# Kernel optimization log

Hardware: AMD Instinct MI355X
Metric: run time of the kernel (lower is better)

Reference implementation:

```python
import jax, jax.numpy as jnp
import numpy as np

N = 100000
F_IN = 128
F_OUT = 128
NNZ = 1_600_000  # avg degree 16


def spmm(rows, cols, vals, X, n):
    """Sparse [n,n] (COO: rows, cols, vals) times dense X [n,d] -> [n,d]."""
    return jax.ops.segment_sum(vals[:, None] * X[cols], rows, num_segments=n)


def setup_inputs() -> dict:
    key = jax.random.key(0)
    ks = jax.random.split(key, 8)
    x = jax.random.normal(ks[0], (N, F_IN), dtype=jnp.float32)
    W = jax.random.normal(ks[1], (F_IN, F_OUT), dtype=jnp.float32) * 0.05
    kernel = jnp.ones((N, 1), dtype=jnp.float32)  # tf.ones_initializer
    phi0_rows = jax.random.randint(ks[2], (NNZ,), 0, N, dtype=jnp.int64)
    phi0_cols = jax.random.randint(ks[3], (NNZ,), 0, N, dtype=jnp.int64)
    phi0_vals = jax.random.uniform(ks[4], (NNZ,), dtype=jnp.float32)
    phi1_rows = jax.random.randint(ks[5], (NNZ,), 0, N, dtype=jnp.int64)
    phi1_cols = jax.random.randint(ks[6], (NNZ,), 0, N, dtype=jnp.int64)
    phi1_vals = jax.random.uniform(ks[7], (NNZ,), dtype=jnp.float32)
    return {
        "x": x, "W": W, "kernel": kernel,
        "phi0_rows": phi0_rows, "phi0_cols": phi0_cols, "phi0_vals": phi0_vals,
        "phi1_rows": phi1_rows, "phi1_cols": phi1_cols, "phi1_vals": phi1_vals,
    }


def reference(x, W, kernel, phi0_rows, phi0_cols, phi0_vals,
              phi1_rows, phi1_cols, phi1_vals):
    # X' = x @ W  (dense feature projection)
    X_prime = x @ W  # [N, F_OUT]
    # X'_t = phi0 @ X'  (SpMM with wavelet basis)
    X_t = spmm(phi0_rows, phi0_cols, phi0_vals, X_prime, N)
    # out = phi1 @ (kernel * X'_t)  (elementwise spectral scaling then SpMM)
    out = spmm(phi1_rows, phi1_cols, phi1_vals, kernel * X_t, N)
    return jax.nn.relu(out)
```

## Files before the change

kernel.cpp:

```cpp
#include <hip/hip_runtime.h>


constexpr int kN = 100000;
constexpr int kF = 128;
constexpr int kNNZ = 1600000;

constexpr int kBuckets = (kN + 255) / 256;
constexpr int kBucketCap = 4608;
constexpr int kChunk = 7168;
constexpr int kChunkBlocks = (kNNZ + kChunk - 1) / kChunk;
constexpr int kSlotsPerMat = kChunkBlocks * kChunk;
constexpr int kDirStride = kBuckets + 1;
constexpr int kTransBlocks = 64;
constexpr int kGemmBlocks = (kN + 127) / 128;
constexpr int kSpmmBlocks512 = kN * 32 / 512;
constexpr int kRowBlocks = kN * 32 / 256;

typedef short bf16x8 __attribute__((ext_vector_type(8)));
typedef float f32x4 __attribute__((ext_vector_type(4)));
typedef unsigned short ushort4v __attribute__((ext_vector_type(4)));

__device__ __forceinline__ unsigned short f32_to_bf16(float f) {
    unsigned int u = __float_as_uint(f);
    u += 0x7fffu + ((u >> 16) & 1u);
    return (unsigned short)(u >> 16);
}
__device__ __forceinline__ float bf16_to_f32(unsigned short h) {
    return __uint_as_float((unsigned int)h << 16);
}

__global__ __launch_bounds__(256) void scatter_transpose(
    const float* __restrict__ W, unsigned short* __restrict__ Wt,
    const int* __restrict__ r0, const int* __restrict__ c0, const float* __restrict__ v0,
    const int* __restrict__ r1, const int* __restrict__ c1, const float* __restrict__ v1,
    unsigned long long* __restrict__ stg, unsigned short* __restrict__ dir) {
    const int t = threadIdx.x;
    if (blockIdx.x < kTransBlocks) {
        const int e = blockIdx.x * 256 + t;
        const int n = e & 127, k = e >> 7;
        Wt[n * 128 + k] = f32_to_bf16(W[e]);
        return;
    }

    __shared__ unsigned long long recs[kChunk];
    __shared__ int hist[kDirStride];
    __shared__ int cur[kDirStride];
    __shared__ int sc2[256];

    const int b = blockIdx.x - kTransBlocks;
    const bool m1 = b >= kChunkBlocks;
    const int cb = m1 ? b - kChunkBlocks : b;
    const int* rows = m1 ? r1 : r0;
    const int* cols = m1 ? c1 : c0;
    const float* vals = m1 ? v1 : v0;
    unsigned long long* dst = stg + (size_t)b * kChunk;
    unsigned short* dirm = dir + (size_t)b * kDirStride;

    for (int i = t; i < kDirStride; i += 256) hist[i] = 0;
    __syncthreads();

    const int base0 = cb * kChunk;
    const int cnt = min(kNNZ - base0, kChunk);

    for (int j = t; j < cnt; j += 256) atomicAdd(&hist[rows[base0 + j] >> 8], 1);
    __syncthreads();

    int s = 0;
    if (t < 196) s = hist[2 * t] + hist[2 * t + 1];
    sc2[t] = (t < 196) ? s : 0;
    __syncthreads();
    #pragma unroll
    for (int off = 1; off < 256; off <<= 1) {
        const int add = (t >= off) ? sc2[t - off] : 0;
        __syncthreads();
        sc2[t] += add;
        __syncthreads();
    }
    if (t < 196) {
        const int ex = sc2[t] - s;
        cur[2 * t] = ex;
        cur[2 * t + 1] = ex + hist[2 * t];
        dirm[2 * t] = (unsigned short)ex;
        dirm[2 * t + 1] = (unsigned short)(ex + hist[2 * t]);
    }
    __syncthreads();

    for (int j = t; j < cnt; j += 256) {
        const int idx = base0 + j;
        const int r = rows[idx];
        const int bk = r >> 8;
        const int pos = atomicAdd(&cur[bk], 1);
        const unsigned int key = ((unsigned int)(r & 255) << 17) | (unsigned int)cols[idx];
        recs[pos] = ((unsigned long long)__float_as_uint(vals[idx]) << 32) | key;
    }
    __syncthreads();

    for (int j = t; j < cnt; j += 256) dst[j] = recs[j];
}

__device__ __forceinline__ void sort_bucket_body(
    char* smem, int bk, int matSel,
    const unsigned long long* __restrict__ stg,
    const unsigned short* __restrict__ dir,
    unsigned long long* __restrict__ sortedG,
    int* __restrict__ rs, int* __restrict__ re) {
    unsigned long long* sorted = (unsigned long long*)smem;
    int* rlen = (int*)(smem + 36864);
    int* gst  = (int*)(smem + 36864 + 896);
    int* hist = (int*)(smem + 36864 + 1792);
    int* sc   = (int*)(smem + 36864 + 2816);
    int* cur  = (int*)(smem + 36864 + 3840);

    const int t = threadIdx.x;
    const unsigned long long* stgm = stg + (matSel ? (size_t)kSlotsPerMat : 0);

    if (t < kChunkBlocks) {
        const unsigned short* dd =
            dir + (size_t)(matSel * kChunkBlocks + t) * kDirStride;
        const int s = dd[bk];
        rlen[t] = dd[bk + 1] - s;
        gst[t] = t * kChunk + s;
    }
    if (t < 256) hist[t] = 0;
    __syncthreads();

    const int g = t >> 5;
    const int lane = t & 31;

    for (int blk = g; blk < kChunkBlocks; blk += 16) {
        const int len = rlen[blk];
        const int gs = gst[blk];
        for (int i = lane; i < len; i += 32) {
            const unsigned int lo = (unsigned int)stgm[gs + i];
            atomicAdd(&hist[(lo >> 17) & 255], 1);
        }
    }
    __syncthreads();

    const int v = (t < 256) ? hist[t] : 0;
    if (t < 256) sc[t] = v;
    __syncthreads();
    #pragma unroll
    for (int off = 1; off < 256; off <<= 1) {
        const int add = (t < 256 && t >= off) ? sc[t - off] : 0;
        __syncthreads();
        if (t < 256) sc[t] += add;
        __syncthreads();
    }
    if (t < 256) cur[t] = sc[t] - v;
    __syncthreads();

    for (int blk = g; blk < kChunkBlocks; blk += 16) {
        const int len = rlen[blk];
        const int gs = gst[blk];
        for (int i = lane; i < len; i += 32) {
            const unsigned long long p = stgm[gs + i];
            const int lrow = (int)(((unsigned int)p >> 17) & 255);
            sorted[atomicAdd(&cur[lrow], 1)] = p;
        }
    }
    __syncthreads();

    const int nrec = sc[255];
    const int bidx = matSel * kBuckets + bk;
    const size_t outBase = (size_t)bidx * kBucketCap;
    for (int j = t; j < nrec; j += 512) sortedG[outBase + j] = sorted[j];
    if (t < 256) {
        const int row = bk * 256 + t;
        if (row < kN) {
            const int rg = matSel * kN + row;
            rs[rg] = (int)outBase + sc[t] - hist[t];
            re[rg] = (int)outBase + sc[t];
        }
    }
}

template <bool ROW_SCALE, bool RELU, bool OUT_BF16>
__device__ __forceinline__ void spmm_row_body(
    int r, int lane,
    const int* __restrict__ rs, const int* __restrict__ re,
    const unsigned long long* __restrict__ rec,
    const float* __restrict__ scale,
    const unsigned short* __restrict__ Xin,
    void* __restrict__ Xout) {
    const int s = rs[r];
    const int e = re[r];

    float4 acc = make_float4(0.f, 0.f, 0.f, 0.f);

    for (int base = s; base < e; base += 32) {
        int cl = 0;
        float vl = 0.f;
        if (base + lane < e) {
            const unsigned long long p = __builtin_nontemporal_load(&rec[base + lane]);
            cl = (int)((unsigned int)p & 0x1FFFF);
            vl = __uint_as_float((unsigned int)(p >> 32));
        }
        const int m4 = (min(32, e - base) + 3) & ~3;
        for (int j = 0; j < m4; j += 4) {
            const int c0 = __shfl(cl, j, 32);
            const int c1 = __shfl(cl, j + 1, 32);
            const int c2 = __shfl(cl, j + 2, 32);
            const int c3 = __shfl(cl, j + 3, 32);
            const float w0 = __shfl(vl, j, 32);
            const float w1 = __shfl(vl, j + 1, 32);
            const float w2 = __shfl(vl, j + 2, 32);
            const float w3 = __shfl(vl, j + 3, 32);
            const ushort4v x0 = *(const ushort4v*)(Xin + (size_t)c0 * kF + lane * 4);
            const ushort4v x1 = *(const ushort4v*)(Xin + (size_t)c1 * kF + lane * 4);
            const ushort4v x2 = *(const ushort4v*)(Xin + (size_t)c2 * kF + lane * 4);
            const ushort4v x3 = *(const ushort4v*)(Xin + (size_t)c3 * kF + lane * 4);
            acc.x = fmaf(w0, bf16_to_f32(x0.x), acc.x);
            acc.y = fmaf(w0, bf16_to_f32(x0.y), acc.y);
            acc.z = fmaf(w0, bf16_to_f32(x0.z), acc.z);
            acc.w = fmaf(w0, bf16_to_f32(x0.w), acc.w);
            acc.x = fmaf(w1, bf16_to_f32(x1.x), acc.x);
            acc.y = fmaf(w1, bf16_to_f32(x1.y), acc.y);
            acc.z = fmaf(w1, bf16_to_f32(x1.z), acc.z);
            acc.w = fmaf(w1, bf16_to_f32(x1.w), acc.w);
            acc.x = fmaf(w2, bf16_to_f32(x2.x), acc.x);
            acc.y = fmaf(w2, bf16_to_f32(x2.y), acc.y);
            acc.z = fmaf(w2, bf16_to_f32(x2.z), acc.z);
            acc.w = fmaf(w2, bf16_to_f32(x2.w), acc.w);
            acc.x = fmaf(w3, bf16_to_f32(x3.x), acc.x);
            acc.y = fmaf(w3, bf16_to_f32(x3.y), acc.y);
            acc.z = fmaf(w3, bf16_to_f32(x3.z), acc.z);
            acc.w = fmaf(w3, bf16_to_f32(x3.w), acc.w);
        }
    }
    if (ROW_SCALE) {
        const float k = scale[r];
        acc.x *= k; acc.y *= k; acc.z *= k; acc.w *= k;
    }
    if (RELU) {
        acc.x = fmaxf(acc.x, 0.f); acc.y = fmaxf(acc.y, 0.f);
        acc.z = fmaxf(acc.z, 0.f); acc.w = fmaxf(acc.w, 0.f);
    }
    if (OUT_BF16) {
        ushort4v o;
        o.x = f32_to_bf16(acc.x); o.y = f32_to_bf16(acc.y);
        o.z = f32_to_bf16(acc.z); o.w = f32_to_bf16(acc.w);
        __builtin_nontemporal_store(
            o, (ushort4v*)((unsigned short*)Xout + (size_t)r * kF + lane * 4));
    } else {
        f32x4 o;
        o.x = acc.x; o.y = acc.y; o.z = acc.z; o.w = acc.w;
        __builtin_nontemporal_store(o, (f32x4*)Xout + (size_t)r * 32 + lane);
    }
}

__global__ __launch_bounds__(512) void sort_gemm(
    const unsigned long long* __restrict__ stg,
    const unsigned short* __restrict__ dir,
    unsigned long long* __restrict__ sortedG,
    int* __restrict__ rs, int* __restrict__ re,
    const float* __restrict__ x, const unsigned short* __restrict__ Wt,
    unsigned short* __restrict__ Xpb) {
    __shared__ __align__(16) char smem[41728];
    const int t = threadIdx.x;

    if (blockIdx.x < kBuckets) {
        sort_bucket_body(smem, blockIdx.x, 0, stg, dir, sortedG, rs, re);
    } else {
        unsigned short* xs = (unsigned short*)smem;
        const int rowBase = (blockIdx.x - kBuckets) * 128;

        {
            const int lrow = t >> 2;
            const int q = t & 3;
            int srow = rowBase + lrow;
            if (srow >= kN) srow = kN - 1;
            const float4* xr = (const float4*)(x + (size_t)srow * kF) + q * 8;
            #pragma unroll
            for (int i = 0; i < 8; ++i) {
                const float4 f = xr[i];
                ushort4v h;
                h.x = f32_to_bf16(f.x); h.y = f32_to_bf16(f.y);
                h.z = f32_to_bf16(f.z); h.w = f32_to_bf16(f.w);
                const int kidx = q * 32 + i * 4;
                *(ushort4v*)&xs[lrow * 128 + (kidx ^ ((lrow & 7) << 3))] = h;
            }
        }
        __syncthreads();

        const int w = t >> 6;
        const int l = t & 63;
        const int lr = l & 15;
        const int lq = l >> 4;

        f32x4 acc[8];
        #pragma unroll
        for (int n = 0; n < 8; ++n) acc[n] = (f32x4){0.f, 0.f, 0.f, 0.f};

        const int arow = w * 16 + lr;
        #pragma unroll
        for (int ks = 0; ks < 4; ++ks) {
            const int akidx = ks * 32 + lq * 8;
            const bf16x8 a = *(const bf16x8*)&xs[arow * 128 + (akidx ^ ((arow & 7) << 3))];
            #pragma unroll
            for (int n = 0; n < 8; ++n) {
                const int bn = n * 16 + lr;
                const bf16x8 b = *(const bf16x8*)(Wt + bn * 128 + akidx);
                acc[n] = __builtin_amdgcn_mfma_f32_16x16x32_bf16(a, b, acc[n], 0, 0, 0);
            }
        }

        #pragma unroll
        for (int j = 0; j < 4; ++j) {
            const int row = rowBase + w * 16 + lq * 4 + j;
            if (row < kN) {
                unsigned short* orow = Xpb + (size_t)row * kF + lr;
                #pragma unroll
                for (int n = 0; n < 8; ++n) orow[n * 16] = f32_to_bf16(acc[n][j]);
            }
        }
    }
}

__global__ __launch_bounds__(512) void sort_spmm(
    const unsigned long long* __restrict__ stg,
    const unsigned short* __restrict__ dir,
    unsigned long long* __restrict__ sortedG,
    int* __restrict__ rs, int* __restrict__ re,
    const float* __restrict__ kern,
    const unsigned short* __restrict__ Xpb,
    unsigned short* __restrict__ Xtb) {
    __shared__ __align__(16) char smem[41728];

    if (blockIdx.x < kBuckets) {
        sort_bucket_body(smem, blockIdx.x, 1, stg, dir, sortedG, rs, re);
    } else {
        const int t = threadIdx.x;
        const int r = (blockIdx.x - kBuckets) * 16 + (t >> 5);
        spmm_row_body<true, false, true>(r, t & 31, rs, re, sortedG, kern, Xpb, Xtb);
    }
}

__global__ __launch_bounds__(256) void spmm_csr(const int* __restrict__ rs,
                                                const int* __restrict__ re,
                                                const unsigned long long* __restrict__ rec,
                                                const unsigned short* __restrict__ Xin,
                                                float* __restrict__ Xout) {
    const int tid = blockIdx.x * 256 + threadIdx.x;
    spmm_row_body<false, true, false>(tid >> 5, tid & 31, rs, re, rec, nullptr,
                                      Xin, Xout);
}

extern "C" void kernel_launch(void* const* d_in, const int* in_sizes, int n_in,
                              void* d_out, int out_size, void* d_ws, size_t ws_size,
                              hipStream_t stream) {
    const float* x    = (const float*)d_in[0];
    const float* W    = (const float*)d_in[1];
    const float* kern = (const float*)d_in[2];
    const int*   p0r  = (const int*)d_in[3];
    const int*   p0c  = (const int*)d_in[4];
    const float* p0v  = (const float*)d_in[5];
    const int*   p1r  = (const int*)d_in[6];
    const int*   p1c  = (const int*)d_in[7];
    const float* p1v  = (const float*)d_in[8];

    unsigned long long* stg = (unsigned long long*)d_out;

    char* w = (char*)d_ws;
    size_t off = 0;
    unsigned short* Xpb = (unsigned short*)(w + off); off += (size_t)kN * kF * 2;
    unsigned short* Xtb = (unsigned short*)(w + off); off += (size_t)kN * kF * 2;
    unsigned short* Wt = (unsigned short*)(w + off);  off += 128 * 128 * 2;
    unsigned short* dir = (unsigned short*)(w + off);
    off += (size_t)2 * kChunkBlocks * kDirStride * 2;
    off = (off + 15) & ~(size_t)15;
    unsigned long long* sortedG = (unsigned long long*)(w + off);
    off += (size_t)2 * kBuckets * kBucketCap * 8;
    int* rs = (int*)(w + off);                        off += (size_t)2 * kN * 4;
    int* re = (int*)(w + off);                        off += (size_t)2 * kN * 4;

    scatter_transpose<<<kTransBlocks + 2 * kChunkBlocks, 256, 0, stream>>>(
        W, Wt, p0r, p0c, p0v, p1r, p1c, p1v, stg, dir);

    sort_gemm<<<kBuckets + kGemmBlocks, 512, 0, stream>>>(
        stg, dir, sortedG, rs, re, x, Wt, Xpb);

    sort_spmm<<<kBuckets + kSpmmBlocks512, 512, 0, stream>>>(
        stg, dir, sortedG, rs, re, kern, Xpb, Xtb);

    spmm_csr<<<kRowBlocks, 256, 0, stream>>>(rs + kN, re + kN, sortedG, Xtb,
                                             (float*)d_out);
}
```

Before: 205.4 us.

## Slice feature matrices into 16-column panels and pack sparse records to 32 bits

The dense intermediates are stored as 8 feature slices of 16 bf16 columns, each contiguous over rows. Each SpMM block now handles one slice for 64 rows, with 8 lanes per row, so that concurrently running blocks gather from a smaller working set with better cache locality. Sparse records shrink from 64-bit (fp32 value) to 32-bit (17-bit column plus fp16 value), halving index traffic. The cost is fp16 rounding of the matrix values, eightfold rereads of the row pointers and records, and narrower 4-byte gathers.

```diff
diff --git a/kernel.cpp b/kernel.cpp
--- a/kernel.cpp
+++ b/kernel.cpp
@@ -1,4 +1,5 @@
 #include <hip/hip_runtime.h>
+#include <hip/hip_fp16.h>
 
 
 constexpr int kN = 100000;
@@ -13,8 +14,10 @@
 constexpr int kDirStride = kBuckets + 1;
 constexpr int kTransBlocks = 64;
 constexpr int kGemmBlocks = (kN + 127) / 128;
-constexpr int kSpmmBlocks512 = kN * 32 / 512;
-constexpr int kRowBlocks = kN * 32 / 256;
+constexpr int kSliceN = 8;
+constexpr int kSliceF = 16;
+constexpr int kSpmmRowGroups = (kN + 63) / 64;
+constexpr int kSpmmBlocksSM = kSliceN * kSpmmRowGroups;
 
 typedef short bf16x8 __attribute__((ext_vector_type(8)));
 typedef float f32x4 __attribute__((ext_vector_type(4)));
@@ -24,9 +27,6 @@
     unsigned int u = __float_as_uint(f);
     u += 0x7fffu + ((u >> 16) & 1u);
     return (unsigned short)(u >> 16);
-}
-__device__ __forceinline__ float bf16_to_f32(unsigned short h) {
-    return __uint_as_float((unsigned int)h << 16);
 }
 
 __global__ __launch_bounds__(256) void scatter_transpose(
@@ -102,7 +102,7 @@
     char* smem, int bk, int matSel,
     const unsigned long long* __restrict__ stg,
     const unsigned short* __restrict__ dir,
-    unsigned long long* __restrict__ sortedG,
+    unsigned int* __restrict__ sortedG,
     int* __restrict__ rs, int* __restrict__ re) {
     unsigned long long* sorted = (unsigned long long*)smem;
     int* rlen = (int*)(smem + 36864);
@@ -164,7 +164,13 @@
     const int nrec = sc[255];
     const int bidx = matSel * kBuckets + bk;
     const size_t outBase = (size_t)bidx * kBucketCap;
-    for (int j = t; j < nrec; j += 512) sortedG[outBase + j] = sorted[j];
+    for (int j = t; j < nrec; j += 512) {
+        const unsigned long long p = sorted[j];
+        const unsigned int col = (unsigned int)p & 0x1FFFFu;
+        const float vv = __uint_as_float((unsigned int)(p >> 32));
+        const unsigned short h = __half_as_ushort(__float2half(vv));
+        sortedG[outBase + j] = col | ((unsigned int)h << 17);
+    }
     if (t < 256) {
         const int row = bk * 256 + t;
         if (row < kN) {
@@ -176,83 +182,69 @@
 }
 
 template <bool ROW_SCALE, bool RELU, bool OUT_BF16>
-__device__ __forceinline__ void spmm_row_body(
-    int r, int lane,
+__device__ __forceinline__ void spmm_slice_body(
+    int slice, int rowBase, int t,
     const int* __restrict__ rs, const int* __restrict__ re,
-    const unsigned long long* __restrict__ rec,
+    const unsigned int* __restrict__ rec,
     const float* __restrict__ scale,
-    const unsigned short* __restrict__ Xin,
+    const unsigned short* __restrict__ Xsm,
     void* __restrict__ Xout) {
-    const int s = rs[r];
-    const int e = re[r];
-
-    float4 acc = make_float4(0.f, 0.f, 0.f, 0.f);
-
-    for (int base = s; base < e; base += 32) {
+    const int r = rowBase + (t >> 3);
+    if (r >= kN) return;
+    const int lane8 = t & 7;
+    const int s0 = rs[r];
+    const int e0 = re[r];
+    const unsigned short* Xs = Xsm + (size_t)slice * kN * kSliceF;
+
+    float a0 = 0.f, a1 = 0.f;
+    for (int base = s0; base < e0; base += 8) {
         int cl = 0;
         float vl = 0.f;
-        if (base + lane < e) {
-            const unsigned long long p = __builtin_nontemporal_load(&rec[base + lane]);
-            cl = (int)((unsigned int)p & 0x1FFFF);
-            vl = __uint_as_float((unsigned int)(p >> 32));
-        }
-        const int m4 = (min(32, e - base) + 3) & ~3;
-        for (int j = 0; j < m4; j += 4) {
-            const int c0 = __shfl(cl, j, 32);
-            const int c1 = __shfl(cl, j + 1, 32);
-            const int c2 = __shfl(cl, j + 2, 32);
-            const int c3 = __shfl(cl, j + 3, 32);
-            const float w0 = __shfl(vl, j, 32);
-            const float w1 = __shfl(vl, j + 1, 32);
-            const float w2 = __shfl(vl, j + 2, 32);
-            const float w3 = __shfl(vl, j + 3, 32);
-            const ushort4v x0 = *(const ushort4v*)(Xin + (size_t)c0 * kF + lane * 4);
-            const ushort4v x1 = *(const ushort4v*)(Xin + (size_t)c1 * kF + lane * 4);
-            const ushort4v x2 = *(const ushort4v*)(Xin + (size_t)c2 * kF + lane * 4);
-            const ushort4v x3 = *(const ushort4v*)(Xin + (size_t)c3 * kF + lane * 4);
-            acc.x = fmaf(w0, bf16_to_f32(x0.x), acc.x);
-            acc.y = fmaf(w0, bf16_to_f32(x0.y), acc.y);
-            acc.z = fmaf(w0, bf16_to_f32(x0.z), acc.z);
-            acc.w = fmaf(w0, bf16_to_f32(x0.w), acc.w);
-            acc.x = fmaf(w1, bf16_to_f32(x1.x), acc.x);
-            acc.y = fmaf(w1, bf16_to_f32(x1.y), acc.y);
-            acc.z = fmaf(w1, bf16_to_f32(x1.z), acc.z);
-            acc.w = fmaf(w1, bf16_to_f32(x1.w), acc.w);
-            acc.x = fmaf(w2, bf16_to_f32(x2.x), acc.x);
-            acc.y = fmaf(w2, bf16_to_f32(x2.y), acc.y);
-            acc.z = fmaf(w2, bf16_to_f32(x2.z), acc.z);
-            acc.w = fmaf(w2, bf16_to_f32(x2.w), acc.w);
-            acc.x = fmaf(w3, bf16_to_f32(x3.x), acc.x);
-            acc.y = fmaf(w3, bf16_to_f32(x3.y), acc.y);
-            acc.z = fmaf(w3, bf16_to_f32(x3.z), acc.z);
-            acc.w = fmaf(w3, bf16_to_f32(x3.w), acc.w);
+        if (base + lane8 < e0) {
+            const unsigned int p = __builtin_nontemporal_load(&rec[base + lane8]);
+            cl = (int)(p & 0x1FFFFu);
+            vl = __half2float(__ushort_as_half((unsigned short)(p >> 17)));
+        }
+        int cc[8];
+        float ww[8];
+        unsigned int xv[8];
+        #pragma unroll
+        for (int q = 0; q < 8; ++q) {
+            cc[q] = __shfl(cl, q, 8);
+            ww[q] = __shfl(vl, q, 8);
+        }
+        #pragma unroll
+        for (int q = 0; q < 8; ++q)
+            xv[q] = *(const unsigned int*)(Xs + (size_t)cc[q] * kSliceF + lane8 * 2);
+        #pragma unroll
+        for (int q = 0; q < 8; ++q) {
+            a0 = fmaf(ww[q], __uint_as_float(xv[q] << 16), a0);
+            a1 = fmaf(ww[q], __uint_as_float(xv[q] & 0xFFFF0000u), a1);
         }
     }
     if (ROW_SCALE) {
         const float k = scale[r];
-        acc.x *= k; acc.y *= k; acc.z *= k; acc.w *= k;
+        a0 *= k; a1 *= k;
     }
     if (RELU) {
-        acc.x = fmaxf(acc.x, 0.f); acc.y = fmaxf(acc.y, 0.f);
-        acc.z = fmaxf(acc.z, 0.f); acc.w = fmaxf(acc.w, 0.f);
+        a0 = fmaxf(a0, 0.f); a1 = fmaxf(a1, 0.f);
     }
     if (OUT_BF16) {
-        ushort4v o;
-        o.x = f32_to_bf16(acc.x); o.y = f32_to_bf16(acc.y);
-        o.z = f32_to_bf16(acc.z); o.w = f32_to_bf16(acc.w);
+        const unsigned int o = ((unsigned int)f32_to_bf16(a1) << 16) | f32_to_bf16(a0);
         __builtin_nontemporal_store(
-            o, (ushort4v*)((unsigned short*)Xout + (size_t)r * kF + lane * 4));
+            o, (unsigned int*)((unsigned short*)Xout +
+                               ((size_t)slice * kN + r) * kSliceF + lane8 * 2));
     } else {
-        f32x4 o;
-        o.x = acc.x; o.y = acc.y; o.z = acc.z; o.w = acc.w;
-        __builtin_nontemporal_store(o, (f32x4*)Xout + (size_t)r * 32 + lane);
+        float* dst = (float*)Xout + (size_t)r * kF + slice * kSliceF + lane8 * 2;
+        __builtin_nontemporal_store(a0, dst);
+        __builtin_nontemporal_store(a1, dst + 1);
     }
 }
 
 __global__ __launch_bounds__(512) void sort_gemm(
     const unsigned long long* __restrict__ stg,
     const unsigned short* __restrict__ dir,
-    unsigned long long* __restrict__ sortedG,
+    unsigned int* __restrict__ sortedG,
     int* __restrict__ rs, int* __restrict__ re,
     const float* __restrict__ x, const unsigned short* __restrict__ Wt,
     unsigned short* __restrict__ Xpb) {
@@ -309,9 +301,9 @@
         for (int j = 0; j < 4; ++j) {
             const int row = rowBase + w * 16 + lq * 4 + j;
             if (row < kN) {
-                unsigned short* orow = Xpb + (size_t)row * kF + lr;
                 #pragma unroll
-                for (int n = 0; n < 8; ++n) orow[n * 16] = f32_to_bf16(acc[n][j]);
+                for (int n = 0; n < 8; ++n)
+                    Xpb[((size_t)n * kN + row) * kSliceF + lr] = f32_to_bf16(acc[n][j]);
             }
         }
     }
@@ -320,7 +312,7 @@
 __global__ __launch_bounds__(512) void sort_spmm(
     const unsigned long long* __restrict__ stg,
     const unsigned short* __restrict__ dir,
-    unsigned long long* __restrict__ sortedG,
+    unsigned int* __restrict__ sortedG,
     int* __restrict__ rs, int* __restrict__ re,
     const float* __restrict__ kern,
     const unsigned short* __restrict__ Xpb,
@@ -330,20 +322,23 @@
     if (blockIdx.x < kBuckets) {
         sort_bucket_body(smem, blockIdx.x, 1, stg, dir, sortedG, rs, re);
     } else {
-        const int t = threadIdx.x;
-        const int r = (blockIdx.x - kBuckets) * 16 + (t >> 5);
-        spmm_row_body<true, false, true>(r, t & 31, rs, re, sortedG, kern, Xpb, Xtb);
-    }
-}
-
-__global__ __launch_bounds__(256) void spmm_csr(const int* __restrict__ rs,
-                                                const int* __restrict__ re,
-                                                const unsigned long long* __restrict__ rec,
-                                                const unsigned short* __restrict__ Xin,
-                                                float* __restrict__ Xout) {
-    const int tid = blockIdx.x * 256 + threadIdx.x;
-    spmm_row_body<false, true, false>(tid >> 5, tid & 31, rs, re, rec, nullptr,
-                                      Xin, Xout);
+        const int sb = blockIdx.x - kBuckets;
+        const int slice = sb & 7;
+        const int rowBase = (sb >> 3) * 64;
+        spmm_slice_body<true, false, true>(slice, rowBase, threadIdx.x,
+                                           rs, re, sortedG, kern, Xpb, Xtb);
+    }
+}
+
+__global__ __launch_bounds__(512) void spmm_out(
+    const int* __restrict__ rs, const int* __restrict__ re,
+    const unsigned int* __restrict__ rec,
+    const unsigned short* __restrict__ Xtb,
+    float* __restrict__ out) {
+    const int slice = blockIdx.x & 7;
+    const int rowBase = (blockIdx.x >> 3) * 64;
+    spmm_slice_body<false, true, false>(slice, rowBase, threadIdx.x,
+                                        rs, re, rec, nullptr, Xtb, out);
 }
 
 extern "C" void kernel_launch(void* const* d_in, const int* in_sizes, int n_in,
@@ -369,8 +364,8 @@
     unsigned short* dir = (unsigned short*)(w + off);
     off += (size_t)2 * kChunkBlocks * kDirStride * 2;
     off = (off + 15) & ~(size_t)15;
-    unsigned long long* sortedG = (unsigned long long*)(w + off);
-    off += (size_t)2 * kBuckets * kBucketCap * 8;
+    unsigned int* sortedG = (unsigned int*)(w + off);
+    off += (size_t)2 * kBuckets * kBucketCap * 4;
     int* rs = (int*)(w + off);                        off += (size_t)2 * kN * 4;
     int* re = (int*)(w + off);                        off += (size_t)2 * kN * 4;
 
@@ -380,9 +375,9 @@
     sort_gemm<<<kBuckets + kGemmBlocks, 512, 0, stream>>>(
         stg, dir, sortedG, rs, re, x, Wt, Xpb);
 
-    sort_spmm<<<kBuckets + kSpmmBlocks512, 512, 0, stream>>>(
+    sort_spmm<<<kBuckets + kSpmmBlocksSM, 512, 0, stream>>>(
         stg, dir, sortedG, rs, re, kern, Xpb, Xtb);
 
-    spmm_csr<<<kRowBlocks, 256, 0, stream>>>(rs + kN, re + kN, sortedG, Xtb,
-                                             (float*)d_out);
-}
+    spmm_out<<<kSpmmBlocksSM, 512, 0, stream>>>(rs + kN, re + kN, sortedG, Xtb,
+                                                (float*)d_out);
+}
```

Result: slower. 326.2 us (+58.9%).
